# Kernel optimization log

Hardware: AMD Instinct MI355X
Metric: run time of the kernel (lower is better)

## Reference

```python
import jax, jax.numpy as jnp
from jax import lax
import numpy as np

CONF_THRES = 0.25
IOU_THRES = 0.45
MAX_OUT = 100  # max_output_boxes_per_class
N_BOXES = 25200  # YOLO 640x640 anchor count


def setup_inputs() -> dict:
    key = jax.random.key(0)
    kb, ks = jax.random.split(key)
    u = jax.random.uniform(kb, (N_BOXES, 4), dtype=jnp.float32)
    # build realistic corner boxes (x1,y1,x2,y2) on a 640x640 canvas
    cx, cy = u[:, 0] * 640.0, u[:, 1] * 640.0
    w = u[:, 2] * 60.0 + 4.0
    h = u[:, 3] * 60.0 + 4.0
    boxes = jnp.stack([cx - w / 2, cy - h / 2, cx + w / 2, cy + h / 2], axis=1)
    scores = jax.random.uniform(ks, (N_BOXES,), dtype=jnp.float32)
    return {"boxes": boxes, "scores": scores}


def _nms_indices(boxes, scores):
    """Greedy NMS. Returns (indices[MAX_OUT] into original boxes, valid[MAX_OUT] mask).
    Confidence filtering (scores > conf_thres) is done by masking to -inf so shapes stay static."""
    n = scores.shape[0]
    s = jnp.where(scores > CONF_THRES, scores, -jnp.inf)
    order = jnp.argsort(-s)               # descending score order
    b = boxes[order]                      # [N,4] sorted boxes
    s = s[order]                          # [N] sorted scores
    area = jnp.maximum(b[:, 2] - b[:, 0], 0.0) * jnp.maximum(b[:, 3] - b[:, 1], 0.0)
    pos = jnp.arange(n)

    def body(i, suppressed):
        keep_i = (~suppressed[i]) & jnp.isfinite(s[i])
        lt = jnp.maximum(b[i, :2], b[:, :2])   # intersection top-left
        rb = jnp.minimum(b[i, 2:], b[:, 2:])   # intersection bottom-right
        wh = jnp.maximum(rb - lt, 0.0)
        inter = wh[:, 0] * wh[:, 1]
        iou = inter / (area[i] + area - inter + 1e-9)
        return suppressed | (keep_i & (pos > i) & (iou > IOU_THRES))

    suppressed = lax.fori_loop(0, n, body, jnp.zeros((n,), bool))
    keep = (~suppressed) & jnp.isfinite(s)
    # pack first MAX_OUT kept (already in score order) into fixed-size output
    rank = jnp.cumsum(keep) - 1
    slot = jnp.where(keep & (rank < MAX_OUT), rank, MAX_OUT)  # overflow/dropped -> slot MAX_OUT
    out_idx = jnp.zeros((MAX_OUT + 1,), jnp.int32).at[slot].set(order.astype(jnp.int32))
    out_valid = jnp.zeros((MAX_OUT + 1,), bool).at[slot].set(keep)
    return out_idx[:MAX_OUT], out_valid[:MAX_OUT]


def reference(boxes, scores):
    idx, valid = _nms_indices(boxes, scores)
    vf = valid.astype(boxes.dtype)
    filtered_boxes = boxes[idx] * vf[:, None]   # zero-padded past the kept count
    filtered_scores = scores[idx] * vf
    return filtered_boxes, filtered_scores
```

## Files before the change

kernel.cpp:

```cpp
#include <hip/hip_runtime.h>
#include <math.h>

#define NB      25200
#define NB4     6300
#define THREADS 1024
#define KV      7
#define NBINS   512
#define CAP     128
#define MAXOUT  100
#define CONF    0.25f
#define PRE     0.98f
#define IOU_T   0.45f
#define NWAVE   16
#define ITEMS_FB 25

typedef unsigned long long u64;
typedef unsigned int u32;

__device__ __forceinline__ bool better(float sa_, int ia_, float sb_, int ib_) {
    return (sb_ > sa_) || (sb_ == sa_ && ib_ < ia_);
}

__global__ __launch_bounds__(THREADS, 1)
void nms_all(const float* __restrict__ boxes,
             const float* __restrict__ scores,
             float* __restrict__ out)
{
    const int tid  = threadIdx.x;
    const int lane = tid & 63;
    const int wv   = tid >> 6;

    __shared__ int    hist[NBINS];
    __shared__ u64    keys[CAP];
    __shared__ float4 sbv[CAP];
    __shared__ float  ss[CAP];
    __shared__ float4 cand_b[CAP];
    __shared__ float  cand_s[CAP];
    __shared__ int    cand_i[CAP];
    __shared__ u64    mat[CAP][2];
    __shared__ int    prank[8][CAP];
    __shared__ int    klist[MAXOUT];
    __shared__ int    s_cnt, s_tbin, s_pack, s_kept;
    __shared__ float  red_v[NWAVE];
    __shared__ int    red_i[NWAVE];
    __shared__ float  live[25600];

    const float4* b4 = (const float4*)boxes;
    const float4* s4 = (const float4*)scores;
    const float binscale = (float)NBINS / (1.0f - PRE);

    float4 sc[KV];
#pragma unroll
    for (int k = 0; k < KV; ++k) {
        const int v = k * THREADS + tid;
        sc[k] = (v < NB4) ? s4[v] : make_float4(-1.f, -1.f, -1.f, -1.f);
    }
    if (tid < NBINS) hist[tid] = 0;
    if (tid == 0) { s_cnt = 0; s_pack = 0; }
    __syncthreads();

    int pack = 0;
#pragma unroll
    for (int k = 0; k < KV; ++k) {
        const float el[4] = {sc[k].x, sc[k].y, sc[k].z, sc[k].w};
#pragma unroll
        for (int e = 0; e < 4; ++e) {
            const float s = el[e];
            if (s > CONF) pack += 0x10000;
            if (s > PRE) {
                pack += 1;
                int b = (int)((s - PRE) * binscale);
                b = b < 0 ? 0 : (b > NBINS - 1 ? NBINS - 1 : b);
                atomicAdd(&hist[b], 1);
            }
        }
    }
#pragma unroll
    for (int off = 1; off < 64; off <<= 1) pack += __shfl_xor(pack, off);
    if (lane == 0) atomicAdd(&s_pack, pack);
    __syncthreads();
    const int total_conf = s_pack >> 16;

    if (tid < 64) {
        int h[8], ls[8];
#pragma unroll
        for (int r = 0; r < 8; ++r) h[r] = hist[lane * 8 + r];
        int acc = 0;
#pragma unroll
        for (int r = 7; r >= 0; --r) { acc += h[r]; ls[r] = acc; }
        u32 inc = (u32)acc;
#pragma unroll
        for (int off = 1; off < 64; off <<= 1) {
            const u32 t = __shfl_down(inc, off);
            if (lane + off < 64) inc += t;
        }
        const int excl = (int)inc - acc;
        int loc = NBINS;
#pragma unroll
        for (int r = 7; r >= 0; --r) { if (ls[r] + excl <= CAP) loc = lane * 8 + r; }
#pragma unroll
        for (int off = 32; off >= 1; off >>= 1) {
            const int t = __shfl_xor(loc, off);
            if (t < loc) loc = t;
        }
        if (lane == 0) s_tbin = loc;
    }
    __syncthreads();
    const int tbin = s_tbin;

#pragma unroll
    for (int k = 0; k < KV; ++k) {
        const int v = k * THREADS + tid;
        const float el[4] = {sc[k].x, sc[k].y, sc[k].z, sc[k].w};
#pragma unroll
        for (int e = 0; e < 4; ++e) {
            const float s = el[e];
            bool pred = false;
            if (s > PRE) {
                int b = (int)((s - PRE) * binscale);
                b = b < 0 ? 0 : (b > NBINS - 1 ? NBINS - 1 : b);
                pred = (b >= tbin);
            }
            if (pred) {
                const int pos = atomicAdd(&s_cnt, 1);
                if (pos < CAP) {
                    const int i = 4 * v + e;
                    cand_s[pos] = s; cand_i[pos] = i; cand_b[pos] = b4[i];
                }
            }
        }
    }
    __syncthreads();
    const int M0 = s_cnt;
    const int M  = (M0 > CAP) ? CAP : M0;

    float cs = 0.f; int ci = 0; float4 cb = make_float4(0.f, 0.f, 0.f, 0.f);
    if (tid < CAP) {
        if (tid < M) { cs = cand_s[tid]; ci = cand_i[tid]; cb = cand_b[tid]; }
        keys[tid] = (tid < M)
            ? (((u64)(~__float_as_uint(cs)) << 32) | (u64)(u32)ci)
            : (0xFFFFFFFF00000000ULL | (u64)tid);
    }
    __syncthreads();

    {
        const int key   = tid & (CAP - 1);
        const int chunk = tid >> 7;
        const u64 myk   = keys[key];
        u64 kb[16];
#pragma unroll
        for (int q = 0; q < 16; ++q) kb[q] = keys[chunk * 16 + q];
        int r = 0;
#pragma unroll
        for (int q = 0; q < 16; ++q) r += (kb[q] < myk) ? 1 : 0;
        prank[chunk][key] = r;
    }
    __syncthreads();
    if (tid < CAP && tid < M) {
        int rank = 0;
#pragma unroll
        for (int c = 0; c < 8; ++c) rank += prank[c][tid];
        sbv[rank] = cb;
        ss[rank]  = cs;
    }
    __syncthreads();

    {
        const int word = wv & 1;
        const int rb   = (wv >> 1) * 16;
        const int jidx = (word << 6) + lane;
        const float4 bj = sbv[jidx];
        const float  aj = fmaxf(bj.z - bj.x, 0.f) * fmaxf(bj.w - bj.y, 0.f);
        const bool   jv = (jidx < M);
        for (int ii = 0; ii < 16; ii += 4) {
            float4 bi[4];
#pragma unroll
            for (int q = 0; q < 4; ++q) bi[q] = sbv[rb + ii + q];
#pragma unroll
            for (int q = 0; q < 4; ++q) {
                const int irow = rb + ii + q;
                const float ai = fmaxf(bi[q].z - bi[q].x, 0.f) * fmaxf(bi[q].w - bi[q].y, 0.f);
                const float ltx = fmaxf(bi[q].x, bj.x);
                const float lty = fmaxf(bi[q].y, bj.y);
                const float rbx = fminf(bi[q].z, bj.z);
                const float rby = fminf(bi[q].w, bj.w);
                const float w_ = fmaxf(rbx - ltx, 0.f);
                const float h_ = fmaxf(rby - lty, 0.f);
                const float inter = w_ * h_;
                const float den = ((ai + aj) - inter) + 1e-9f;
                const bool pred = jv && (irow < M) && (jidx > irow) && (inter > IOU_T * den);
                const u64 bal = __ballot(pred);
                if (lane == 0) mat[irow][word] = bal;
            }
        }
    }
    __syncthreads();

    if (tid == 0) {
        u64 r0 = 0, r1 = 0;
        int kept = 0;
        for (int base = 0; base < M && kept < MAXOUT; base += 8) {
            u64 rw[8][2];
#pragma unroll
            for (int q = 0; q < 8; ++q) { rw[q][0] = mat[base + q][0]; rw[q][1] = mat[base + q][1]; }
#pragma unroll
            for (int q = 0; q < 8; ++q) {
                const int i = base + q;
                if (i >= M || kept >= MAXOUT) break;
                const u64 cur = (i < 64) ? r0 : r1;
                if (!((cur >> (i & 63)) & 1ULL)) {
                    klist[kept++] = i;
                    if (kept == MAXOUT) break;
                    r0 |= rw[q][0]; r1 |= rw[q][1];
                }
            }
        }
        s_kept = kept;
    }
    __syncthreads();

    const int kept = s_kept;
    const bool need_fb = (M0 > CAP) || (kept < MAXOUT && M0 < total_conf);
    if (!need_fb) {
        if (tid < MAXOUT) {
            float4 bb = make_float4(0.f, 0.f, 0.f, 0.f);
            float  sc_ = 0.f;
            if (tid < kept) { const int j = klist[tid]; bb = sbv[j]; sc_ = ss[j]; }
            out[4*tid+0] = bb.x; out[4*tid+1] = bb.y;
            out[4*tid+2] = bb.z; out[4*tid+3] = bb.w;
            out[4*MAXOUT + tid] = sc_;
        }
        return;
    }

    if (tid < 25600 - NB) live[NB + tid] = -INFINITY;
    for (int k = 0; k < ITEMS_FB; ++k) {
        const int i = k * THREADS + tid;
        if (i < NB) {
            const float s0 = scores[i];
            live[i] = (s0 > CONF) ? s0 : -INFINITY;
        }
    }
    __syncthreads();
    for (int r = 0; r < MAXOUT; ++r) {
        float lm = -INFINITY; int li = 0x7fffffff;
        for (int k = 0; k < ITEMS_FB; ++k) {
            const int i = k * THREADS + tid;
            const float v = live[i];
            if (v > lm) { lm = v; li = i; }
        }
        float rv = lm; int ri = li;
#pragma unroll
        for (int off = 32; off >= 1; off >>= 1) {
            const float ov = __shfl_xor(rv, off);
            const int   oi = __shfl_xor(ri, off);
            if (better(rv, ri, ov, oi)) { rv = ov; ri = oi; }
        }
        __syncthreads();
        if (lane == 0) { red_v[wv] = rv; red_i[wv] = ri; }
        __syncthreads();
        float wval = red_v[0]; int widx = red_i[0];
#pragma unroll
        for (int j = 1; j < NWAVE; ++j) {
            const float v = red_v[j]; const int i2 = red_i[j];
            if (better(wval, widx, v, i2)) { wval = v; widx = i2; }
        }
        if (!(wval > -1e38f)) {
            if (tid == 0) {
                out[4*r+0]=0.f; out[4*r+1]=0.f; out[4*r+2]=0.f; out[4*r+3]=0.f;
                out[4*MAXOUT + r] = 0.f;
            }
            continue;
        }
        const float4 wb = b4[widx];
        if (tid == 0) {
            out[4*r+0]=wb.x; out[4*r+1]=wb.y; out[4*r+2]=wb.z; out[4*r+3]=wb.w;
            out[4*MAXOUT + r] = wval;
        }
        const float warea = fmaxf(wb.z - wb.x, 0.f) * fmaxf(wb.w - wb.y, 0.f);
        for (int k = 0; k < ITEMS_FB; ++k) {
            const int i = k * THREADS + tid;
            if (i < NB) {
                const float4 bb = b4[i];
                const float area = fmaxf(bb.z - bb.x, 0.f) * fmaxf(bb.w - bb.y, 0.f);
                const float ltx = fmaxf(bb.x, wb.x);
                const float lty = fmaxf(bb.y, wb.y);
                const float rbx = fminf(bb.z, wb.z);
                const float rby = fminf(bb.w, wb.w);
                const float w  = fmaxf(rbx - ltx, 0.f);
                const float h  = fmaxf(rby - lty, 0.f);
                const float inter = w * h;
                const float den = ((warea + area) - inter) + 1e-9f;
                if (inter > IOU_T * den || i == widx) live[i] = -INFINITY;
            }
        }
        __syncthreads();
    }
}

extern "C" void kernel_launch(void* const* d_in, const int* in_sizes, int n_in,
                              void* d_out, int out_size, void* d_ws, size_t ws_size,
                              hipStream_t stream) {
    const float* boxes  = (const float*)d_in[0];
    const float* scores = (const float*)d_in[1];
    float* out = (float*)d_out;
    nms_all<<<dim3(1), dim3(THREADS), 0, stream>>>(boxes, scores, out);
}
```

Measured before the change: 77.12 us.

## Stage pre-threshold candidates during histogram pass and simplify rank sort

During the histogram pass, every score above the pre-threshold is appended to a shared staging buffer together with its box, so the box gathers overlap the histogram work. The second scan over all register scores is replaced by a pass over only the staged entries, which writes sort keys directly. The chunked partial-rank sort and its extra barriers become a single per-thread rank loop over 128 keys, and the output store is vectorized. In exchange the first pass pays for box loads and an extra atomic per candidate, and a new fallback condition covers staging-buffer overflow.

```diff
diff --git a/kernel.cpp b/kernel.cpp
--- a/kernel.cpp
+++ b/kernel.cpp
@@ -7,6 +7,7 @@
 #define KV      7
 #define NBINS   512
 #define CAP     128
+#define PCAP    768
 #define MAXOUT  100
 #define CONF    0.25f
 #define PRE     0.98f
@@ -36,11 +37,12 @@
     __shared__ float  ss[CAP];
     __shared__ float4 cand_b[CAP];
     __shared__ float  cand_s[CAP];
-    __shared__ int    cand_i[CAP];
+    __shared__ float4 pre_b[PCAP];
+    __shared__ float  pre_s[PCAP];
+    __shared__ int    pre_i[PCAP];
     __shared__ u64    mat[CAP][2];
-    __shared__ int    prank[8][CAP];
     __shared__ int    klist[MAXOUT];
-    __shared__ int    s_cnt, s_tbin, s_pack, s_kept;
+    __shared__ int    s_cnt, s_tbin, s_pack, s_pre, s_kept;
     __shared__ float  red_v[NWAVE];
     __shared__ int    red_i[NWAVE];
     __shared__ float  live[25600];
@@ -56,12 +58,14 @@
         sc[k] = (v < NB4) ? s4[v] : make_float4(-1.f, -1.f, -1.f, -1.f);
     }
     if (tid < NBINS) hist[tid] = 0;
-    if (tid == 0) { s_cnt = 0; s_pack = 0; }
+    if (tid < CAP)   keys[tid] = 0xFFFFFFFF00000000ULL | (u64)tid;
+    if (tid == 0) { s_cnt = 0; s_pack = 0; s_pre = 0; }
     __syncthreads();
 
     int pack = 0;
 #pragma unroll
     for (int k = 0; k < KV; ++k) {
+        const int v = k * THREADS + tid;
         const float el[4] = {sc[k].x, sc[k].y, sc[k].z, sc[k].w};
 #pragma unroll
         for (int e = 0; e < 4; ++e) {
@@ -72,6 +76,11 @@
                 int b = (int)((s - PRE) * binscale);
                 b = b < 0 ? 0 : (b > NBINS - 1 ? NBINS - 1 : b);
                 atomicAdd(&hist[b], 1);
+                const int pos = atomicAdd(&s_pre, 1);
+                if (pos < PCAP) {
+                    const int i = 4 * v + e;
+                    pre_s[pos] = s; pre_i[pos] = i; pre_b[pos] = b4[i];
+                }
             }
         }
     }
@@ -80,6 +89,7 @@
     if (lane == 0) atomicAdd(&s_pack, pack);
     __syncthreads();
     const int total_conf = s_pack >> 16;
+    const int pre_cnt = s_pre;
 
     if (tid < 64) {
         int h[8], ls[8];
@@ -108,24 +118,18 @@
     __syncthreads();
     const int tbin = s_tbin;
 
-#pragma unroll
-    for (int k = 0; k < KV; ++k) {
-        const int v = k * THREADS + tid;
-        const float el[4] = {sc[k].x, sc[k].y, sc[k].z, sc[k].w};
-#pragma unroll
-        for (int e = 0; e < 4; ++e) {
-            const float s = el[e];
-            bool pred = false;
-            if (s > PRE) {
-                int b = (int)((s - PRE) * binscale);
-                b = b < 0 ? 0 : (b > NBINS - 1 ? NBINS - 1 : b);
-                pred = (b >= tbin);
-            }
-            if (pred) {
+    {
+        const int Mpre = (pre_cnt < PCAP) ? pre_cnt : PCAP;
+        if (tid < Mpre) {
+            const float s = pre_s[tid];
+            int b = (int)((s - PRE) * binscale);
+            b = b < 0 ? 0 : (b > NBINS - 1 ? NBINS - 1 : b);
+            if (b >= tbin) {
                 const int pos = atomicAdd(&s_cnt, 1);
                 if (pos < CAP) {
-                    const int i = 4 * v + e;
-                    cand_s[pos] = s; cand_i[pos] = i; cand_b[pos] = b4[i];
+                    keys[pos]   = ((u64)(~__float_as_uint(s)) << 32) | (u64)(u32)pre_i[tid];
+                    cand_s[pos] = s;
+                    cand_b[pos] = pre_b[tid];
                 }
             }
         }
@@ -134,34 +138,18 @@
     const int M0 = s_cnt;
     const int M  = (M0 > CAP) ? CAP : M0;
 
-    float cs = 0.f; int ci = 0; float4 cb = make_float4(0.f, 0.f, 0.f, 0.f);
     if (tid < CAP) {
-        if (tid < M) { cs = cand_s[tid]; ci = cand_i[tid]; cb = cand_b[tid]; }
-        keys[tid] = (tid < M)
-            ? (((u64)(~__float_as_uint(cs)) << 32) | (u64)(u32)ci)
-            : (0xFFFFFFFF00000000ULL | (u64)tid);
-    }
-    __syncthreads();
-
-    {
-        const int key   = tid & (CAP - 1);
-        const int chunk = tid >> 7;
-        const u64 myk   = keys[key];
-        u64 kb[16];
-#pragma unroll
-        for (int q = 0; q < 16; ++q) kb[q] = keys[chunk * 16 + q];
-        int r = 0;
-#pragma unroll
-        for (int q = 0; q < 16; ++q) r += (kb[q] < myk) ? 1 : 0;
-        prank[chunk][key] = r;
-    }
-    __syncthreads();
-    if (tid < CAP && tid < M) {
+        const u64 myk = keys[tid];
         int rank = 0;
 #pragma unroll
-        for (int c = 0; c < 8; ++c) rank += prank[c][tid];
-        sbv[rank] = cb;
-        ss[rank]  = cs;
+        for (int q0 = 0; q0 < CAP; q0 += 16) {
+            u64 kq[16];
+#pragma unroll
+            for (int q = 0; q < 16; ++q) kq[q] = keys[q0 + q];
+#pragma unroll
+            for (int q = 0; q < 16; ++q) rank += (kq[q] < myk) ? 1 : 0;
+        }
+        if (tid < M) { sbv[rank] = cand_b[tid]; ss[rank] = cand_s[tid]; }
     }
     __syncthreads();
 
@@ -220,14 +208,13 @@
     __syncthreads();
 
     const int kept = s_kept;
-    const bool need_fb = (M0 > CAP) || (kept < MAXOUT && M0 < total_conf);
+    const bool need_fb = (M0 > CAP) || (pre_cnt > PCAP) || (kept < MAXOUT && M0 < total_conf);
     if (!need_fb) {
         if (tid < MAXOUT) {
             float4 bb = make_float4(0.f, 0.f, 0.f, 0.f);
             float  sc_ = 0.f;
             if (tid < kept) { const int j = klist[tid]; bb = sbv[j]; sc_ = ss[j]; }
-            out[4*tid+0] = bb.x; out[4*tid+1] = bb.y;
-            out[4*tid+2] = bb.z; out[4*tid+3] = bb.w;
+            ((float4*)out)[tid] = bb;
             out[4*MAXOUT + tid] = sc_;
         }
         return;
```

Result: slower. 81.87 us (+6.2%).
